# Kernel optimization log

Hardware: AMD Instinct MI355X
Metric: run time of the kernel (lower is better)

## Reference

```python
import jax, jax.numpy as jnp
import numpy as np

K = 5
TAU = 0.5
N = 8192
IN_DIM = 128
OUT_DIM = 128


def setup_inputs() -> dict:
    key = jax.random.key(0)
    k1, k2, k3 = jax.random.split(key, 3)
    x = jax.random.normal(k1, (N, IN_DIM), dtype=jnp.float32)
    laplacian = jax.random.normal(k2, (N, N), dtype=jnp.float32) / np.sqrt(N)
    # xavier-uniform-like init for theta (K, in_dim, out_dim)
    limit = np.sqrt(6.0 / (IN_DIM + OUT_DIM))
    theta = jax.random.uniform(k3, (K, IN_DIM, OUT_DIM), dtype=jnp.float32,
                               minval=-limit, maxval=limit)
    return {"x": x, "laplacian": laplacian, "theta": theta}


def _cheb_coeff(k_order: int, tau: float) -> jnp.ndarray:
    # c_k = (2/K) * exp(-tau * cos(pi*(k+0.5)/K)), Chebyshev-Gauss nodes
    ks = jnp.arange(k_order, dtype=jnp.float32)
    x_k = jnp.cos(jnp.pi * (ks + 0.5) / k_order)
    return (2.0 / k_order) * jnp.exp(-tau * x_k)


def reference(x, laplacian, theta):
    coeff = _cheb_coeff(K, TAU)  # (K,)
    # Chebyshev recurrence: T_0 = x, T_1 = L x, T_k = 2 L T_{k-1} - T_{k-2}
    tx_prev, tx_curr = x, laplacian @ x
    tx_list = [tx_prev, tx_curr]
    for _ in range(2, K):
        tx_next = 2.0 * (laplacian @ tx_curr) - tx_prev
        tx_list.append(tx_next)
        tx_prev, tx_curr = tx_curr, tx_next
    tx_stack = jnp.stack(tx_list, axis=0)  # (K, N, in_dim)
    return jnp.einsum('kni,kio,k->no', tx_stack, theta, coeff)
```

## Files before the change

kernel.cpp:

```cpp
#include <hip/hip_runtime.h>
#include <hip/hip_bf16.h>
#include <cmath>

#define NROWS 8192
#define DIM   128
#define KDIM  8192
#define BM    64
#define BN    128
#define BK    64
#define SPLITK 4
#define KCHUNK (KDIM / SPLITK)
#define GITERS (KCHUNK / BK)
#define MTILES (NROWS / BM)
#define KBLKS  (KDIM / BK)
#define LDSTRIDE 80

typedef __bf16 bf16_t;
typedef __bf16 bf16x8 __attribute__((ext_vector_type(8)));
typedef float  f32x4  __attribute__((ext_vector_type(4)));


__device__ __forceinline__ void async16(const void* g, void* l) {
    __builtin_amdgcn_global_load_lds(
        (const __attribute__((address_space(1))) unsigned int*)g,
        (__attribute__((address_space(3))) unsigned int*)l, 16, 0, 0);
}

__global__ void k_theta(const float* __restrict__ th, bf16_t* __restrict__ out,
                        float c0, float c1, float c2, float c3, float c4) {
    int idx = blockIdx.x * 256 + threadIdx.x;
    int k = idx >> 14;
    int o = (idx >> 7) & 127;
    int i = idx & 127;
    float c = (k == 0) ? c0 : (k == 1) ? c1 : (k == 2) ? c2 : (k == 3) ? c3 : c4;
    out[idx] = (bf16_t)(c * th[(k << 14) + (i << 7) + o]);
}

template <int MODE>
__global__ __launch_bounds__(256, 2)
void k_gemm(const void* __restrict__ Ap, const bf16_t* __restrict__ Bt,
            float* __restrict__ partial, bf16_t* __restrict__ Lbf_out) {
    __shared__ __align__(16) bf16_t As[2][BM * BK];
    __shared__ __align__(16) bf16_t Bs[2][BN * BK];

    const int t     = threadIdx.x;
    const int mTile = blockIdx.x & (MTILES - 1);
    const int s     = blockIdx.x >> 7;
    const int mb    = mTile * BM;
    const int sKB   = s * (KCHUNK / BK);
    const int rgA   = mb >> 3;
    const int wave = t >> 6, lane = t & 63;
    const int wM = (wave & 1) * 32;
    const int wN = (wave >> 1) * 64;
    const int lm = lane & 15, lk = lane >> 4;
    const int lrow = lane >> 3;
    const int p0   = lane & 7;
    const int lsrc = p0 ^ lrow;

    f32x4 acc[2][4];
#pragma unroll
    for (int a = 0; a < 2; ++a)
#pragma unroll
        for (int b = 0; b < 4; ++b) acc[a][b] = (f32x4)0.0f;

    float4 RA[2][2][2];

    auto stageB = [&](int kk, int buf) {
        const int kblk = sKB + kk;
#pragma unroll
        for (int i = 0; i < 4; ++i) {
            const int fg = wave * 4 + i;
            async16(Bt + (((size_t)fg * KBLKS + kblk) * 64 + lane) * 8,
                    &Bs[buf][(wave * 32 + i * 8) * BK]);
        }
    };
    auto stageA0 = [&](int kk, int buf) {
        const int kblk = sKB + kk;
#pragma unroll
        for (int j = 0; j < 2; ++j) {
            const int rg = rgA + wave * 2 + j;
            async16((const bf16_t*)Ap + (((size_t)rg * KBLKS + kblk) * 64 + lane) * 8,
                    &As[buf][(wave * 16 + j * 8) * BK]);
        }
    };
    auto loadA2 = [&](int kk, int st) {
        const int k0 = s * KCHUNK + kk * BK;
#pragma unroll
        for (int j = 0; j < 2; ++j) {
            const int row = mb + wave * 16 + j * 8 + lrow;
            const float* base = (const float*)Ap + (size_t)row * KDIM + k0 + lsrc * 8;
            RA[st][j][0] = *(const float4*)base;
            RA[st][j][1] = *(const float4*)(base + 4);
        }
    };
    auto writeA2 = [&](int kk, int buf, int st) {
        const int kblk = sKB + kk;
#pragma unroll
        for (int j = 0; j < 2; ++j) {
            bf16x8 v;
            v[0] = (bf16_t)RA[st][j][0].x; v[1] = (bf16_t)RA[st][j][0].y;
            v[2] = (bf16_t)RA[st][j][0].z; v[3] = (bf16_t)RA[st][j][0].w;
            v[4] = (bf16_t)RA[st][j][1].x; v[5] = (bf16_t)RA[st][j][1].y;
            v[6] = (bf16_t)RA[st][j][1].z; v[7] = (bf16_t)RA[st][j][1].w;
            *(bf16x8*)(&As[buf][(wave * 16 + j * 8 + lrow) * BK + p0 * 8]) = v;
            const int rg = rgA + wave * 2 + j;
            *(bf16x8*)(Lbf_out + (((size_t)rg * KBLKS + kblk) * 64 + lane) * 8) = v;
        }
    };

    auto compute = [&](int buf) {
#pragma unroll
        for (int ko = 0; ko < 2; ++ko) {
            const int csX = (ko * 4 + lk) ^ (lm & 7);
            bf16x8 af[2], bfr[4];
#pragma unroll
            for (int tm = 0; tm < 2; ++tm)
                af[tm] = *(const bf16x8*)(&As[buf][(wM + tm * 16 + lm) * BK + csX * 8]);
#pragma unroll
            for (int tn = 0; tn < 4; ++tn)
                bfr[tn] = *(const bf16x8*)(&Bs[buf][(wN + tn * 16 + lm) * BK + csX * 8]);
#pragma unroll
            for (int tm = 0; tm < 2; ++tm)
#pragma unroll
                for (int tn = 0; tn < 4; ++tn)
                    acc[tm][tn] = __builtin_amdgcn_mfma_f32_16x16x32_bf16(
                        af[tm], bfr[tn], acc[tm][tn], 0, 0, 0);
        }
    };

    if (MODE == 0) {
        stageA0(0, 0); stageB(0, 0);
        __syncthreads();
        for (int kk = 0; kk < GITERS; ++kk) {
            const int buf = kk & 1;
            if (kk + 1 < GITERS) { stageA0(kk + 1, buf ^ 1); stageB(kk + 1, buf ^ 1); }
            compute(buf);
            __syncthreads();
        }
    } else {
        loadA2(0, 0); stageB(0, 0);
        for (int kk = 0; kk < GITERS; ++kk) {
            const int buf = kk & 1;
            writeA2(kk, buf, kk & 1);
            __syncthreads();
            if (kk + 1 < GITERS) { loadA2(kk + 1, (kk + 1) & 1); stageB(kk + 1, buf ^ 1); }
            compute(buf);
        }
    }

    float* pOut = partial + (size_t)s * NROWS * DIM;
#pragma unroll
    for (int tm = 0; tm < 2; ++tm)
#pragma unroll
        for (int tn = 0; tn < 4; ++tn)
#pragma unroll
            for (int r = 0; r < 4; ++r) {
                const int row = mb + wM + tm * 16 + lk * 4 + r;
                const int col = wN + tn * 16 + lm;
                pOut[(size_t)row * DIM + col] = acc[tm][tn][r];
            }
}

template <int MODE>
__global__ void k_combine(const float* __restrict__ src, const float* __restrict__ prev,
                          float* __restrict__ f32dst, bf16_t* __restrict__ tbf,
                          bf16_t* __restrict__ bt) {
    __shared__ bf16_t tl[128 * 24];
    const size_t S = (size_t)NROWS * DIM;
    const int t  = threadIdx.x;
    const int n0 = blockIdx.x * 16;
    const int nl = t >> 4;
    const int dp = (t & 15) * 8;
    const int n  = n0 + nl;

    float y[8];
    if (MODE == 0) {
        float4 a = *(const float4*)(src + (size_t)n * DIM + dp);
        float4 b = *(const float4*)(src + (size_t)n * DIM + dp + 4);
        y[0] = a.x; y[1] = a.y; y[2] = a.z; y[3] = a.w;
        y[4] = b.x; y[5] = b.y; y[6] = b.z; y[7] = b.w;
    } else {
#pragma unroll
        for (int j = 0; j < 8; ++j) y[j] = 0.0f;
#pragma unroll
        for (int ss = 0; ss < SPLITK; ++ss) {
            const float* p = src + (size_t)ss * S + (size_t)n * DIM + dp;
            float4 a = *(const float4*)p;
            float4 b = *(const float4*)(p + 4);
            y[0] += a.x; y[1] += a.y; y[2] += a.z; y[3] += a.w;
            y[4] += b.x; y[5] += b.y; y[6] += b.z; y[7] += b.w;
        }
        if (MODE == 2) {
            float4 a = *(const float4*)(prev + (size_t)n * DIM + dp);
            float4 b = *(const float4*)(prev + (size_t)n * DIM + dp + 4);
            y[0] = 2.0f * y[0] - a.x; y[1] = 2.0f * y[1] - a.y;
            y[2] = 2.0f * y[2] - a.z; y[3] = 2.0f * y[3] - a.w;
            y[4] = 2.0f * y[4] - b.x; y[5] = 2.0f * y[5] - b.y;
            y[6] = 2.0f * y[6] - b.z; y[7] = 2.0f * y[7] - b.w;
        }
    }
    if (f32dst) {
        float4 a, b;
        a.x = y[0]; a.y = y[1]; a.z = y[2]; a.w = y[3];
        b.x = y[4]; b.y = y[5]; b.z = y[6]; b.w = y[7];
        *(float4*)(f32dst + (size_t)n * DIM + dp) = a;
        *(float4*)(f32dst + (size_t)n * DIM + dp + 4) = b;
    }
    bf16x8 v;
#pragma unroll
    for (int j = 0; j < 8; ++j) v[j] = (bf16_t)y[j];
    *(bf16x8*)(tbf + (size_t)n * DIM + dp) = v;
    if (bt) {
#pragma unroll
        for (int j = 0; j < 8; ++j) tl[(dp + j) * 24 + nl] = v[j];
        __syncthreads();
        const int d = t >> 1;
        const int h = (t & 1) * 8;
        bf16x8 w = *(const bf16x8*)(&tl[d * 24 + h]);
        const int c    = ((n0 + h) >> 3) & 7;
        const int lane = (d & 7) * 8 + (c ^ (d & 7));
        const size_t a16 = ((size_t)(d >> 3) * KBLKS + (n0 >> 6)) * 64 + lane;
        *(bf16x8*)(bt + a16 * 8) = w;
    }
}

__global__ __launch_bounds__(256, 2)
void k_proj(const bf16_t* __restrict__ T, const bf16_t* __restrict__ W,
            float* __restrict__ out) {
    __shared__ __align__(16) bf16_t As[64 * LDSTRIDE];
    __shared__ __align__(16) bf16_t Bs[128 * LDSTRIDE];

    const int t  = threadIdx.x;
    const int mb = blockIdx.x * 64;
    const int wave = t >> 6, lane = t & 63;
    const int wM = (wave & 1) * 32;
    const int wN = (wave >> 1) * 64;
    const int lm = lane & 15, lk = lane >> 4;
    const int arow = t >> 3;
    const int asc  = t & 7;
    const size_t S = (size_t)NROWS * DIM;

    f32x4 acc[2][4];
#pragma unroll
    for (int a = 0; a < 2; ++a)
#pragma unroll
        for (int b = 0; b < 4; ++b) acc[a][b] = (f32x4)0.0f;

    bf16x8 aR[2], bR[4];

    auto loadT = [&](int it) {
        const int seg = it >> 1;
        const int h   = (it & 1) * 64;
#pragma unroll
        for (int rep = 0; rep < 2; ++rep) {
            const int r = rep * 32 + arow;
            aR[rep] = *(const bf16x8*)(T + (size_t)seg * S +
                        (size_t)(mb + r) * DIM + h + asc * 8);
        }
#pragma unroll
        for (int rep = 0; rep < 4; ++rep) {
            const int o = rep * 32 + arow;
            bR[rep] = *(const bf16x8*)(W + seg * 16384 + o * 128 + h + asc * 8);
        }
    };
    auto storeT = [&]() {
#pragma unroll
        for (int rep = 0; rep < 2; ++rep) {
            const int r = rep * 32 + arow;
            *(bf16x8*)(&As[r * LDSTRIDE + asc * 8]) = aR[rep];
        }
#pragma unroll
        for (int rep = 0; rep < 4; ++rep) {
            const int o = rep * 32 + arow;
            *(bf16x8*)(&Bs[o * LDSTRIDE + asc * 8]) = bR[rep];
        }
    };

    loadT(0);
    for (int it = 0; it < 10; ++it) {
        __syncthreads();
        storeT();
        __syncthreads();
        if (it + 1 < 10) loadT(it + 1);
#pragma unroll
        for (int ko = 0; ko < 2; ++ko) {
            bf16x8 af[2], bfr[4];
#pragma unroll
            for (int tm = 0; tm < 2; ++tm)
                af[tm] = *(const bf16x8*)(&As[(wM + tm * 16 + lm) * LDSTRIDE +
                                              (ko * 4 + lk) * 8]);
#pragma unroll
            for (int tn = 0; tn < 4; ++tn)
                bfr[tn] = *(const bf16x8*)(&Bs[(wN + tn * 16 + lm) * LDSTRIDE +
                                               (ko * 4 + lk) * 8]);
#pragma unroll
            for (int tm = 0; tm < 2; ++tm)
#pragma unroll
                for (int tn = 0; tn < 4; ++tn)
                    acc[tm][tn] = __builtin_amdgcn_mfma_f32_16x16x32_bf16(
                        af[tm], bfr[tn], acc[tm][tn], 0, 0, 0);
        }
    }
#pragma unroll
    for (int tm = 0; tm < 2; ++tm)
#pragma unroll
        for (int tn = 0; tn < 4; ++tn)
#pragma unroll
            for (int r = 0; r < 4; ++r) {
                const int row = mb + wM + tm * 16 + lk * 4 + r;
                const int col = wN + tn * 16 + lm;
                out[(size_t)row * DIM + col] = acc[tm][tn][r];
            }
}

extern "C" void kernel_launch(void* const* d_in, const int* in_sizes, int n_in,
                              void* d_out, int out_size, void* d_ws, size_t ws_size,
                              hipStream_t stream) {
    const float* x  = nullptr;
    const float* L  = nullptr;
    const float* th = nullptr;
    for (int i = 0; i < n_in; ++i) {
        if (in_sizes[i] == NROWS * KDIM)       L  = (const float*)d_in[i];
        else if (in_sizes[i] == NROWS * DIM)   x  = (const float*)d_in[i];
        else if (in_sizes[i] == 5 * DIM * DIM) th = (const float*)d_in[i];
    }
    float* out = (float*)d_out;

    const size_t S = (size_t)NROWS * DIM;
    char* ws = (char*)d_ws;
    size_t off = 0;
    auto alloc = [&](size_t bytes) {
        void* p = ws + off;
        off = (off + bytes + 255) & ~(size_t)255;
        return p;
    };
    bf16_t* Tbf     = (bf16_t*)alloc(5 * S * 2);
    bf16_t* Bt      = (bf16_t*)alloc(5 * S * 2);
    float*  Tf32    = (float*)alloc(2 * S * 4);
    bf16_t* thT     = (bf16_t*)alloc(5 * 128 * 128 * 2);
    float*  partial = (float*)alloc((size_t)SPLITK * S * 4);
    bf16_t* Lbf     = (bf16_t*)alloc((size_t)NROWS * KDIM * 2);
    if (off > ws_size) return;

    float c[5];
    for (int k = 0; k < 5; ++k)
        c[k] = (float)((2.0 / 5.0) * exp(-0.5 * cos(M_PI * (k + 0.5) / 5.0)));

    dim3 blk(256);
    k_theta<<<320, blk, 0, stream>>>(th, thT, c[0], c[1], c[2], c[3], c[4]);
    k_combine<0><<<512, blk, 0, stream>>>(x, nullptr, nullptr, Tbf, Bt);

    for (int j = 1; j <= 4; ++j) {
        const bf16_t* Bj = Bt + (size_t)(j - 1) * S;
        if (j == 1)
            k_gemm<2><<<MTILES * SPLITK, blk, 0, stream>>>(L, Bj, partial, Lbf);
        else
            k_gemm<0><<<MTILES * SPLITK, blk, 0, stream>>>(Lbf, Bj, partial, nullptr);
        bf16_t* tbf = Tbf + (size_t)j * S;
        bf16_t* bt  = (j < 4) ? Bt + (size_t)j * S : nullptr;
        if (j == 1)
            k_combine<1><<<512, blk, 0, stream>>>(partial, nullptr, Tf32 + S, tbf, bt);
        else if (j == 2)
            k_combine<2><<<512, blk, 0, stream>>>(partial, x, Tf32, tbf, bt);
        else if (j == 3)
            k_combine<2><<<512, blk, 0, stream>>>(partial, Tf32 + S, Tf32 + S, tbf, bt);
        else
            k_combine<2><<<512, blk, 0, stream>>>(partial, Tf32, nullptr, tbf, nullptr);
    }
    k_proj<<<128, blk, 0, stream>>>(Tbf, thT, out);
}
```

Before: 593.5 us.

## Split L conversion into standalone kernel and triple-buffer GEMM with async LDS loads

Moves the fp32-to-bf16 conversion of the Laplacian out of the first GEMM into a dedicated grid-stride conversion kernel, so every GEMM iteration uses one uniform async-load path. The GEMM main loop becomes a 3-stage LDS pipeline with explicit vmcnt waits and barriers, and MFMA sections are given raised wave priority. The goal is to hide global-load latency better and remove the register-staged conversion from the GEMM. In exchange, L is streamed through an extra pass and LDS use rises by half, which may lower occupancy.

```diff
diff --git a/kernel.cpp b/kernel.cpp
--- a/kernel.cpp
+++ b/kernel.cpp
@@ -13,6 +13,7 @@
 #define GITERS (KCHUNK / BK)
 #define MTILES (NROWS / BM)
 #define KBLKS  (KDIM / BK)
+#define NBUF   3
 #define LDSTRIDE 80
 
 typedef __bf16 bf16_t;
@@ -36,12 +37,33 @@
     out[idx] = (bf16_t)(c * th[(k << 14) + (i << 7) + o]);
 }
 
-template <int MODE>
+__global__ __launch_bounds__(256)
+void k_convert(const float* __restrict__ L, bf16_t* __restrict__ Lbf) {
+    const int lane = threadIdx.x & 63;
+    const int lrow = lane >> 3;
+    const int p    = lane & 7;
+    const int c    = p ^ lrow;
+    const int nWaves = gridDim.x * 4;
+    const int TOT = (NROWS / 8) * KBLKS;
+    for (int w = blockIdx.x * 4 + (threadIdx.x >> 6); w < TOT; w += nWaves) {
+        const int rg   = w >> 7;
+        const int kblk = w & (KBLKS - 1);
+        const int row  = rg * 8 + lrow;
+        const float* src = L + (size_t)row * KDIM + kblk * 64 + c * 8;
+        float4 a = *(const float4*)src;
+        float4 b = *(const float4*)(src + 4);
+        bf16x8 v;
+        v[0] = (bf16_t)a.x; v[1] = (bf16_t)a.y; v[2] = (bf16_t)a.z; v[3] = (bf16_t)a.w;
+        v[4] = (bf16_t)b.x; v[5] = (bf16_t)b.y; v[6] = (bf16_t)b.z; v[7] = (bf16_t)b.w;
+        *(bf16x8*)(Lbf + (((size_t)rg * KBLKS + kblk) * 64 + lane) * 8) = v;
+    }
+}
+
 __global__ __launch_bounds__(256, 2)
-void k_gemm(const void* __restrict__ Ap, const bf16_t* __restrict__ Bt,
-            float* __restrict__ partial, bf16_t* __restrict__ Lbf_out) {
-    __shared__ __align__(16) bf16_t As[2][BM * BK];
-    __shared__ __align__(16) bf16_t Bs[2][BN * BK];
+void k_gemm(const bf16_t* __restrict__ A, const bf16_t* __restrict__ Bt,
+            float* __restrict__ partial) {
+    __shared__ __align__(16) bf16_t As[NBUF][BM * BK];
+    __shared__ __align__(16) bf16_t Bs[NBUF][BN * BK];
 
     const int t     = threadIdx.x;
     const int mTile = blockIdx.x & (MTILES - 1);
@@ -53,9 +75,6 @@
     const int wM = (wave & 1) * 32;
     const int wN = (wave >> 1) * 64;
     const int lm = lane & 15, lk = lane >> 4;
-    const int lrow = lane >> 3;
-    const int p0   = lane & 7;
-    const int lsrc = p0 ^ lrow;
 
     f32x4 acc[2][4];
 #pragma unroll
@@ -63,10 +82,14 @@
 #pragma unroll
         for (int b = 0; b < 4; ++b) acc[a][b] = (f32x4)0.0f;
 
-    float4 RA[2][2][2];
-
-    auto stageB = [&](int kk, int buf) {
+    auto stage = [&](int kk, int buf) {
         const int kblk = sKB + kk;
+#pragma unroll
+        for (int j = 0; j < 2; ++j) {
+            const int rg = rgA + wave * 2 + j;
+            async16(A + (((size_t)rg * KBLKS + kblk) * 64 + lane) * 8,
+                    &As[buf][(wave * 16 + j * 8) * BK]);
+        }
 #pragma unroll
         for (int i = 0; i < 4; ++i) {
             const int fg = wave * 4 + i;
@@ -74,39 +97,6 @@
                     &Bs[buf][(wave * 32 + i * 8) * BK]);
         }
     };
-    auto stageA0 = [&](int kk, int buf) {
-        const int kblk = sKB + kk;
-#pragma unroll
-        for (int j = 0; j < 2; ++j) {
-            const int rg = rgA + wave * 2 + j;
-            async16((const bf16_t*)Ap + (((size_t)rg * KBLKS + kblk) * 64 + lane) * 8,
-                    &As[buf][(wave * 16 + j * 8) * BK]);
-        }
-    };
-    auto loadA2 = [&](int kk, int st) {
-        const int k0 = s * KCHUNK + kk * BK;
-#pragma unroll
-        for (int j = 0; j < 2; ++j) {
-            const int row = mb + wave * 16 + j * 8 + lrow;
-            const float* base = (const float*)Ap + (size_t)row * KDIM + k0 + lsrc * 8;
-            RA[st][j][0] = *(const float4*)base;
-            RA[st][j][1] = *(const float4*)(base + 4);
-        }
-    };
-    auto writeA2 = [&](int kk, int buf, int st) {
-        const int kblk = sKB + kk;
-#pragma unroll
-        for (int j = 0; j < 2; ++j) {
-            bf16x8 v;
-            v[0] = (bf16_t)RA[st][j][0].x; v[1] = (bf16_t)RA[st][j][0].y;
-            v[2] = (bf16_t)RA[st][j][0].z; v[3] = (bf16_t)RA[st][j][0].w;
-            v[4] = (bf16_t)RA[st][j][1].x; v[5] = (bf16_t)RA[st][j][1].y;
-            v[6] = (bf16_t)RA[st][j][1].z; v[7] = (bf16_t)RA[st][j][1].w;
-            *(bf16x8*)(&As[buf][(wave * 16 + j * 8 + lrow) * BK + p0 * 8]) = v;
-            const int rg = rgA + wave * 2 + j;
-            *(bf16x8*)(Lbf_out + (((size_t)rg * KBLKS + kblk) * 64 + lane) * 8) = v;
-        }
-    };
 
     auto compute = [&](int buf) {
 #pragma unroll
@@ -119,34 +109,37 @@
 #pragma unroll
             for (int tn = 0; tn < 4; ++tn)
                 bfr[tn] = *(const bf16x8*)(&Bs[buf][(wN + tn * 16 + lm) * BK + csX * 8]);
+            __builtin_amdgcn_s_setprio(1);
 #pragma unroll
             for (int tm = 0; tm < 2; ++tm)
 #pragma unroll
                 for (int tn = 0; tn < 4; ++tn)
                     acc[tm][tn] = __builtin_amdgcn_mfma_f32_16x16x32_bf16(
                         af[tm], bfr[tn], acc[tm][tn], 0, 0, 0);
-        }
-    };
-
-    if (MODE == 0) {
-        stageA0(0, 0); stageB(0, 0);
-        __syncthreads();
-        for (int kk = 0; kk < GITERS; ++kk) {
-            const int buf = kk & 1;
-            if (kk + 1 < GITERS) { stageA0(kk + 1, buf ^ 1); stageB(kk + 1, buf ^ 1); }
-            compute(buf);
-            __syncthreads();
-        }
-    } else {
-        loadA2(0, 0); stageB(0, 0);
-        for (int kk = 0; kk < GITERS; ++kk) {
-            const int buf = kk & 1;
-            writeA2(kk, buf, kk & 1);
-            __syncthreads();
-            if (kk + 1 < GITERS) { loadA2(kk + 1, (kk + 1) & 1); stageB(kk + 1, buf ^ 1); }
-            compute(buf);
-        }
-    }
+            __builtin_amdgcn_s_setprio(0);
+        }
+    };
+
+    stage(0, 0); stage(1, 1); stage(2, 2);
+
+    for (int kk = 0; kk < GITERS - 2; ++kk) {
+        const int buf = kk % NBUF;
+        asm volatile("s_waitcnt vmcnt(12)" ::: "memory");
+        __builtin_amdgcn_s_barrier();
+        __builtin_amdgcn_sched_barrier(0);
+        compute(buf);
+        __builtin_amdgcn_sched_barrier(0);
+        __builtin_amdgcn_s_barrier();
+        if (kk < GITERS - 3) stage(kk + 3, buf);
+    }
+    asm volatile("s_waitcnt vmcnt(6)" ::: "memory");
+    __builtin_amdgcn_s_barrier();
+    __builtin_amdgcn_sched_barrier(0);
+    compute((GITERS - 2) % NBUF);
+    asm volatile("s_waitcnt vmcnt(0)" ::: "memory");
+    __builtin_amdgcn_s_barrier();
+    __builtin_amdgcn_sched_barrier(0);
+    compute((GITERS - 1) % NBUF);
 
     float* pOut = partial + (size_t)s * NROWS * DIM;
 #pragma unroll
@@ -348,14 +341,12 @@
 
     dim3 blk(256);
     k_theta<<<320, blk, 0, stream>>>(th, thT, c[0], c[1], c[2], c[3], c[4]);
+    k_convert<<<2048, blk, 0, stream>>>(L, Lbf);
     k_combine<0><<<512, blk, 0, stream>>>(x, nullptr, nullptr, Tbf, Bt);
 
     for (int j = 1; j <= 4; ++j) {
         const bf16_t* Bj = Bt + (size_t)(j - 1) * S;
-        if (j == 1)
-            k_gemm<2><<<MTILES * SPLITK, blk, 0, stream>>>(L, Bj, partial, Lbf);
-        else
-            k_gemm<0><<<MTILES * SPLITK, blk, 0, stream>>>(Lbf, Bj, partial, nullptr);
+        k_gemm<<<MTILES * SPLITK, blk, 0, stream>>>(Lbf, Bj, partial);
         bf16_t* tbf = Tbf + (size_t)j * S;
         bf16_t* bt  = (j < 4) ? Bt + (size_t)j * S : nullptr;
         if (j == 1)
```

New measurement: 560.2 us. -5.6%, faster.

## Replace LDS-staged GEMM with direct register loads and triple-buffered fragments

Applied to the files above, without the earlier changes.

The Laplacian GEMM no longer stages A and B tiles through LDS with async global-to-LDS copies and swizzled blocked layouts. Each wave now loads its MFMA fragments straight from plain row-major global memory into registers, using a three-deep software pipeline. Split-K doubles to 8, block indexing is reordered so split slices of one row tile are adjacent, and launch bounds allow three blocks per CU. The transposed B operand written by the combine kernel becomes plain row-major. This removes LDS traffic and barriers, at the cost of duplicate global reads across waves, narrower per-row access segments, and more partial-sum traffic.

```diff
diff --git a/kernel.cpp b/kernel.cpp
--- a/kernel.cpp
+++ b/kernel.cpp
@@ -7,24 +7,15 @@
 #define KDIM  8192
 #define BM    64
 #define BN    128
-#define BK    64
-#define SPLITK 4
+#define SPLITK 8
 #define KCHUNK (KDIM / SPLITK)
-#define GITERS (KCHUNK / BK)
+#define HSTEPS (KCHUNK / 32)
 #define MTILES (NROWS / BM)
-#define KBLKS  (KDIM / BK)
 #define LDSTRIDE 80
 
 typedef __bf16 bf16_t;
 typedef __bf16 bf16x8 __attribute__((ext_vector_type(8)));
 typedef float  f32x4  __attribute__((ext_vector_type(4)));
-
-
-__device__ __forceinline__ void async16(const void* g, void* l) {
-    __builtin_amdgcn_global_load_lds(
-        (const __attribute__((address_space(1))) unsigned int*)g,
-        (__attribute__((address_space(3))) unsigned int*)l, 16, 0, 0);
-}
 
 __global__ void k_theta(const float* __restrict__ th, bf16_t* __restrict__ out,
                         float c0, float c1, float c2, float c3, float c4) {
@@ -36,26 +27,27 @@
     out[idx] = (bf16_t)(c * th[(k << 14) + (i << 7) + o]);
 }
 
-template <int MODE>
-__global__ __launch_bounds__(256, 2)
+struct Frag { bf16x8 a0, a1, b0, b1, b2, b3; };
+
+template <int CVT>
+__global__ __launch_bounds__(256, 3)
 void k_gemm(const void* __restrict__ Ap, const bf16_t* __restrict__ Bt,
             float* __restrict__ partial, bf16_t* __restrict__ Lbf_out) {
-    __shared__ __align__(16) bf16_t As[2][BM * BK];
-    __shared__ __align__(16) bf16_t Bs[2][BN * BK];
-
     const int t     = threadIdx.x;
-    const int mTile = blockIdx.x & (MTILES - 1);
-    const int s     = blockIdx.x >> 7;
+    const int s     = blockIdx.x & (SPLITK - 1);
+    const int mTile = blockIdx.x >> 3;
     const int mb    = mTile * BM;
-    const int sKB   = s * (KCHUNK / BK);
-    const int rgA   = mb >> 3;
     const int wave = t >> 6, lane = t & 63;
     const int wM = (wave & 1) * 32;
     const int wN = (wave >> 1) * 64;
     const int lm = lane & 15, lk = lane >> 4;
-    const int lrow = lane >> 3;
-    const int p0   = lane & 7;
-    const int lsrc = p0 ^ lrow;
+    const int kbase = s * KCHUNK + lk * 8;
+    const int rowA  = mb + wM + lm;
+
+    const bf16_t* bP = Bt + (size_t)(wN + lm) * KDIM + kbase;
+    const bf16_t* aP = (const bf16_t*)Ap + (size_t)rowA * KDIM + kbase;
+    const float*  aF = (const float*)Ap + (size_t)rowA * KDIM + kbase;
+    bf16_t*       wP = CVT ? (Lbf_out + (size_t)rowA * KDIM + kbase) : nullptr;
 
     f32x4 acc[2][4];
 #pragma unroll
@@ -63,90 +55,53 @@
 #pragma unroll
         for (int b = 0; b < 4; ++b) acc[a][b] = (f32x4)0.0f;
 
-    float4 RA[2][2][2];
-
-    auto stageB = [&](int kk, int buf) {
-        const int kblk = sKB + kk;
-#pragma unroll
-        for (int i = 0; i < 4; ++i) {
-            const int fg = wave * 4 + i;
-            async16(Bt + (((size_t)fg * KBLKS + kblk) * 64 + lane) * 8,
-                    &Bs[buf][(wave * 32 + i * 8) * BK]);
-        }
-    };
-    auto stageA0 = [&](int kk, int buf) {
-        const int kblk = sKB + kk;
-#pragma unroll
-        for (int j = 0; j < 2; ++j) {
-            const int rg = rgA + wave * 2 + j;
-            async16((const bf16_t*)Ap + (((size_t)rg * KBLKS + kblk) * 64 + lane) * 8,
-                    &As[buf][(wave * 16 + j * 8) * BK]);
-        }
-    };
-    auto loadA2 = [&](int kk, int st) {
-        const int k0 = s * KCHUNK + kk * BK;
-#pragma unroll
-        for (int j = 0; j < 2; ++j) {
-            const int row = mb + wave * 16 + j * 8 + lrow;
-            const float* base = (const float*)Ap + (size_t)row * KDIM + k0 + lsrc * 8;
-            RA[st][j][0] = *(const float4*)base;
-            RA[st][j][1] = *(const float4*)(base + 4);
-        }
-    };
-    auto writeA2 = [&](int kk, int buf, int st) {
-        const int kblk = sKB + kk;
-#pragma unroll
-        for (int j = 0; j < 2; ++j) {
-            bf16x8 v;
-            v[0] = (bf16_t)RA[st][j][0].x; v[1] = (bf16_t)RA[st][j][0].y;
-            v[2] = (bf16_t)RA[st][j][0].z; v[3] = (bf16_t)RA[st][j][0].w;
-            v[4] = (bf16_t)RA[st][j][1].x; v[5] = (bf16_t)RA[st][j][1].y;
-            v[6] = (bf16_t)RA[st][j][1].z; v[7] = (bf16_t)RA[st][j][1].w;
-            *(bf16x8*)(&As[buf][(wave * 16 + j * 8 + lrow) * BK + p0 * 8]) = v;
-            const int rg = rgA + wave * 2 + j;
-            *(bf16x8*)(Lbf_out + (((size_t)rg * KBLKS + kblk) * 64 + lane) * 8) = v;
-        }
-    };
-
-    auto compute = [&](int buf) {
-#pragma unroll
-        for (int ko = 0; ko < 2; ++ko) {
-            const int csX = (ko * 4 + lk) ^ (lm & 7);
-            bf16x8 af[2], bfr[4];
-#pragma unroll
-            for (int tm = 0; tm < 2; ++tm)
-                af[tm] = *(const bf16x8*)(&As[buf][(wM + tm * 16 + lm) * BK + csX * 8]);
-#pragma unroll
-            for (int tn = 0; tn < 4; ++tn)
-                bfr[tn] = *(const bf16x8*)(&Bs[buf][(wN + tn * 16 + lm) * BK + csX * 8]);
-#pragma unroll
-            for (int tm = 0; tm < 2; ++tm)
-#pragma unroll
-                for (int tn = 0; tn < 4; ++tn)
-                    acc[tm][tn] = __builtin_amdgcn_mfma_f32_16x16x32_bf16(
-                        af[tm], bfr[tn], acc[tm][tn], 0, 0, 0);
-        }
-    };
-
-    if (MODE == 0) {
-        stageA0(0, 0); stageB(0, 0);
-        __syncthreads();
-        for (int kk = 0; kk < GITERS; ++kk) {
-            const int buf = kk & 1;
-            if (kk + 1 < GITERS) { stageA0(kk + 1, buf ^ 1); stageB(kk + 1, buf ^ 1); }
-            compute(buf);
-            __syncthreads();
-        }
-    } else {
-        loadA2(0, 0); stageB(0, 0);
-        for (int kk = 0; kk < GITERS; ++kk) {
-            const int buf = kk & 1;
-            writeA2(kk, buf, kk & 1);
-            __syncthreads();
-            if (kk + 1 < GITERS) { loadA2(kk + 1, (kk + 1) & 1); stageB(kk + 1, buf ^ 1); }
-            compute(buf);
-        }
-    }
+    auto loadF = [&](int h, Frag& f) {
+        const int off = h * 32;
+        if (CVT) {
+            float4 x0 = *(const float4*)(aF + off);
+            float4 x1 = *(const float4*)(aF + off + 4);
+            float4 y0 = *(const float4*)(aF + (size_t)16 * KDIM + off);
+            float4 y1 = *(const float4*)(aF + (size_t)16 * KDIM + off + 4);
+            bf16x8 va, vb;
+            va[0] = (bf16_t)x0.x; va[1] = (bf16_t)x0.y; va[2] = (bf16_t)x0.z; va[3] = (bf16_t)x0.w;
+            va[4] = (bf16_t)x1.x; va[5] = (bf16_t)x1.y; va[6] = (bf16_t)x1.z; va[7] = (bf16_t)x1.w;
+            vb[0] = (bf16_t)y0.x; vb[1] = (bf16_t)y0.y; vb[2] = (bf16_t)y0.z; vb[3] = (bf16_t)y0.w;
+            vb[4] = (bf16_t)y1.x; vb[5] = (bf16_t)y1.y; vb[6] = (bf16_t)y1.z; vb[7] = (bf16_t)y1.w;
+            f.a0 = va; f.a1 = vb;
+            if (wave < 2) {
+                *(bf16x8*)(wP + off) = va;
+                *(bf16x8*)(wP + (size_t)16 * KDIM + off) = vb;
+            }
+        } else {
+            f.a0 = *(const bf16x8*)(aP + off);
+            f.a1 = *(const bf16x8*)(aP + (size_t)16 * KDIM + off);
+        }
+        f.b0 = *(const bf16x8*)(bP + off);
+        f.b1 = *(const bf16x8*)(bP + (size_t)16 * KDIM + off);
+        f.b2 = *(const bf16x8*)(bP + (size_t)32 * KDIM + off);
+        f.b3 = *(const bf16x8*)(bP + (size_t)48 * KDIM + off);
+    };
+    auto mma = [&](const Frag& f) {
+        acc[0][0] = __builtin_amdgcn_mfma_f32_16x16x32_bf16(f.a0, f.b0, acc[0][0], 0, 0, 0);
+        acc[0][1] = __builtin_amdgcn_mfma_f32_16x16x32_bf16(f.a0, f.b1, acc[0][1], 0, 0, 0);
+        acc[0][2] = __builtin_amdgcn_mfma_f32_16x16x32_bf16(f.a0, f.b2, acc[0][2], 0, 0, 0);
+        acc[0][3] = __builtin_amdgcn_mfma_f32_16x16x32_bf16(f.a0, f.b3, acc[0][3], 0, 0, 0);
+        acc[1][0] = __builtin_amdgcn_mfma_f32_16x16x32_bf16(f.a1, f.b0, acc[1][0], 0, 0, 0);
+        acc[1][1] = __builtin_amdgcn_mfma_f32_16x16x32_bf16(f.a1, f.b1, acc[1][1], 0, 0, 0);
+        acc[1][2] = __builtin_amdgcn_mfma_f32_16x16x32_bf16(f.a1, f.b2, acc[1][2], 0, 0, 0);
+        acc[1][3] = __builtin_amdgcn_mfma_f32_16x16x32_bf16(f.a1, f.b3, acc[1][3], 0, 0, 0);
+    };
+
+    Frag f0, f1, f2;
+    loadF(0, f0); loadF(1, f1);
+#pragma unroll
+    for (int it = 0; it < (HSTEPS - 2) / 3; ++it) {
+        const int h = 2 + it * 3;
+        loadF(h,     f2); mma(f0);
+        loadF(h + 1, f0); mma(f1);
+        loadF(h + 2, f1); mma(f2);
+    }
+    mma(f0); mma(f1);
 
     float* pOut = partial + (size_t)s * NROWS * DIM;
 #pragma unroll
@@ -217,10 +172,7 @@
         const int d = t >> 1;
         const int h = (t & 1) * 8;
         bf16x8 w = *(const bf16x8*)(&tl[d * 24 + h]);
-        const int c    = ((n0 + h) >> 3) & 7;
-        const int lane = (d & 7) * 8 + (c ^ (d & 7));
-        const size_t a16 = ((size_t)(d >> 3) * KBLKS + (n0 >> 6)) * 64 + lane;
-        *(bf16x8*)(bt + a16 * 8) = w;
+        *(bf16x8*)(bt + (size_t)d * NROWS + n0 + h) = w;
     }
 }
 
@@ -353,7 +305,7 @@
     for (int j = 1; j <= 4; ++j) {
         const bf16_t* Bj = Bt + (size_t)(j - 1) * S;
         if (j == 1)
-            k_gemm<2><<<MTILES * SPLITK, blk, 0, stream>>>(L, Bj, partial, Lbf);
+            k_gemm<1><<<MTILES * SPLITK, blk, 0, stream>>>(L, Bj, partial, Lbf);
         else
             k_gemm<0><<<MTILES * SPLITK, blk, 0, stream>>>(Lbf, Bj, partial, nullptr);
         bf16_t* tbf = Tbf + (size_t)j * S;
```

Result: slower. 812.0 us (+36.8%).
